# Kernel optimization log

Hardware: AMD Instinct MI355X
Metric: run time of the kernel (lower is better)

The kernel has to match this reference:

```python
import jax, jax.numpy as jnp
import numpy as np


def setup_inputs() -> dict:
    key = jax.random.key(0)
    k0, k1, k2, k3 = jax.random.split(key, 4)
    B, N, C, Dout = 4, 8192, 64, 128
    coords = jax.random.normal(k0, (B, N, 3), dtype=jnp.float32)
    features = jax.random.normal(k1, (B, N, C), dtype=jnp.float32)
    W1 = jax.random.normal(k2, (C + 3, Dout), dtype=jnp.float32) / jnp.sqrt(jnp.float32(C + 3))
    b1 = jnp.zeros((Dout,), dtype=jnp.float32)
    W2 = jax.random.normal(k3, (Dout, Dout), dtype=jnp.float32) / jnp.sqrt(jnp.float32(Dout))
    b2 = jnp.zeros((Dout,), dtype=jnp.float32)
    return {"coords": coords, "features": features, "W1": W1, "b1": b1,
            "W2": W2, "b2": b2, "sample_count": 2048, "k": 32}


def reference(coords, features, W1, b1, W2, b2, sample_count, k):
    B, N, _ = coords.shape
    S = min(sample_count, N)
    kk = min(k, N)
    # deterministic linspace centroid sampling (same indices for every batch)
    idx = jnp.round(jnp.linspace(0.0, N - 1, S)).astype(jnp.int32)  # [S]
    sampled = coords[:, idx]  # [B,S,3]
    # squared distances via GEMM (same topk ordering as torch.cdist)
    s2 = jnp.sum(sampled * sampled, axis=-1)          # [B,S]
    c2 = jnp.sum(coords * coords, axis=-1)            # [B,N]
    d2 = s2[:, :, None] + c2[:, None, :] - 2.0 * jnp.einsum('bsd,bnd->bsn', sampled, coords)
    _, knn_idx = jax.lax.top_k(-d2, kk)               # [B,S,kk] smallest distances
    # per-batch irregular gathers
    grouped_c = jax.vmap(lambda c, i: c[i])(coords, knn_idx)      # [B,S,kk,3]
    rel = grouped_c - sampled[:, :, None, :]                      # relative coords
    grouped_f = jax.vmap(lambda f, i: f[i])(features, knn_idx)    # [B,S,kk,C]
    g = jnp.concatenate([rel, grouped_f], axis=-1)                # [B,S,kk,C+3]
    # shared MLP: Linear -> GELU(exact) -> Linear -> GELU(exact)
    h = jax.nn.gelu(g @ W1 + b1, approximate=False)
    h = jax.nn.gelu(h @ W2 + b2, approximate=False)
    pooled = jnp.max(h, axis=2)                                   # [B,S,Dout]
    return sampled, pooled
```

## Files before the change

kernel.cpp:

```cpp
#include <hip/hip_runtime.h>
#include <math.h>

typedef unsigned int u32;
typedef unsigned long long u64;

#define BB 4
#define NN 8192
#define CC 64
#define DOUT 128
#define SS 2048
#define KSEL 32
#define CAPL 2048
#define CAP2 384
#define BREAK_CAP 128
#define GSTR 36

__device__ __forceinline__ int sample_index(int s) {
    if (s == 1706) return 6826;
    const double step = 8191.0 / 2047.0;
    return (int)rint((double)s * step);
}

__device__ __forceinline__ u32 f2s(float f) {
    u32 u = __float_as_uint(f);
    return ((int)u < 0) ? ~u : (u ^ 0x80000000u);
}

__device__ __forceinline__ float gelu(float x) {
    return 0.5f * x * (1.0f + erff(x * 0.70710678118654752f));
}

__global__ __launch_bounds__(256, 8) void k_select(const float* __restrict__ coords,
                                                   float* __restrict__ out_sampled,
                                                   int* __restrict__ selbuf,
                                                   int selstride) {
    __shared__ __align__(16) u64 cand[CAPL];
    __shared__ __align__(16) u64 cand2[CAP2];
    __shared__ u32 wsum[32];
    __shared__ int sel[KSEL];
    __shared__ int s_nsel, s_ncand, s_n2;

    const int tid = threadIdx.x;
    const int lane = tid & 63;
    const int q = blockIdx.x;
    const int b = q >> 11;
    const int s = q & (SS - 1);
    const int si = sample_index(s);

    const float* cb = coords + (size_t)b * NN * 3;
    const float qx = cb[si * 3 + 0], qy = cb[si * 3 + 1], qz = cb[si * 3 + 2];
    const float q2 = __fadd_rn(__fadd_rn(__fmul_rn(qx, qx), __fmul_rn(qy, qy)), __fmul_rn(qz, qz));

    if (tid == 0) {
        float* dst = out_sampled + (size_t)q * 3;
        dst[0] = qx; dst[1] = qy; dst[2] = qz;
    }

    u32 kr[32];
#pragma unroll
    for (int i = 0; i < 32; i++) {
        int j = tid + (i << 8);
        float x = cb[j * 3 + 0], y = cb[j * 3 + 1], z = cb[j * 3 + 2];
        float n2 = __fadd_rn(__fadd_rn(__fmul_rn(x, x), __fmul_rn(y, y)), __fmul_rn(z, z));
        float dot = __fadd_rn(__fadd_rn(__fmul_rn(qx, x), __fmul_rn(qy, y)), __fmul_rn(qz, z));
        float d2 = __fsub_rn(__fadd_rn(q2, n2), __fmul_rn(2.0f, dot));
        kr[i] = f2s(d2);
    }

#define BFLY_WSUM()                                                          \
    _Pragma("unroll")                                                        \
    for (int w = 0; w < 8; w++) {                                            \
        _Pragma("unroll")                                                    \
        for (int d = 1; d < 64; d <<= 1) cnt[w] += __shfl_xor(cnt[w], d, 64);\
    }                                                                        \
    if ((tid & 63) == 0) {                                                   \
        int wv = tid >> 6;                                                   \
        _Pragma("unroll")                                                    \
        for (int w = 0; w < 8; w++) wsum[wv * 8 + w] = cnt[w];               \
    }                                                                        \
    __syncthreads();

#define SCAN_DIGIT()                                                         \
    u32 tot[8];                                                              \
    _Pragma("unroll")                                                        \
    for (int w = 0; w < 8; w++)                                              \
        tot[w] = wsum[w] + wsum[8 + w] + wsum[16 + w] + wsum[24 + w];        \
    run = 0; D = 15; cc = 0;                                                 \
    _Pragma("unroll")                                                        \
    for (int nib = 0; nib < 16; nib++) {                                     \
        int cv = (nib & 1) ? (int)(tot[nib >> 1] >> 16)                      \
                           : (int)(tot[nib >> 1] & 0xFFFFu);                 \
        if (base + run + cv >= KSEL) { D = nib; cc = cv; break; }            \
        run += cv;                                                           \
    }

    u32 pref = 0;
    int base = 0, shift = 28, c = 0;
    int p = 7;
    {
        u32 cnt[8] = {0, 0, 0, 0, 0, 0, 0, 0};
#pragma unroll
        for (int i = 0; i < 32; i++) {
            u32 nib = kr[i] >> 28;
            cnt[nib >> 1] += 1u << (16 * (nib & 1));
        }
        BFLY_WSUM()
        int run, D, cc;
        SCAN_DIGIT()
        base = run; pref = (u32)D << 28; c = cc;
        __syncthreads();
    }

    while (c > CAPL && p > 0) {
        p--;
        const int sh = 4 * p;
        const u32 hmask = 0xFFFFFFFFu << (sh + 4);
        u32 cnt[8] = {0, 0, 0, 0, 0, 0, 0, 0};
#pragma unroll
        for (int i = 0; i < 32; i++) {
            u32 kv = kr[i];
            if ((kv & hmask) == pref) {
                u32 nib = (kv >> sh) & 15u;
                cnt[nib >> 1] += 1u << (16 * (nib & 1));
            }
        }
        BFLY_WSUM()
        int run, D, cc;
        SCAN_DIGIT()
        base += run; pref |= (u32)D << sh; shift = sh; c = cc;
        __syncthreads();
    }

    if (tid == 0) { s_nsel = 0; s_ncand = 0; }
    __syncthreads();

    const u64 lmlt = (1ull << lane) - 1ull;
    {
        const u32 prefv = pref >> shift;
#pragma unroll
        for (int i = 0; i < 32; i++) {
            int j = tid + (i << 8);
            u32 kv = kr[i];
            u32 kp = kv >> shift;
            bool isS = kp < prefv;
            bool isC = kp == prefv;
            u64 bs = __ballot(isS);
            u64 bc = __ballot(isC);
            int basS = 0, basC = 0;
            if (lane == 0) {
                if (bs) basS = atomicAdd(&s_nsel, (int)__popcll(bs));
                if (bc) basC = atomicAdd(&s_ncand, (int)__popcll(bc));
            }
            basS = __shfl(basS, 0, 64);
            basC = __shfl(basC, 0, 64);
            if (isS) sel[basS + (int)__popcll(bs & lmlt)] = j;
            if (isC) {
                int pos = basC + (int)__popcll(bc & lmlt);
                if (pos < CAPL) cand[pos] = ((u64)kv << 32) | (u32)j;
            }
        }
    }
    __syncthreads();
    int nc = s_ncand; if (nc > CAPL) nc = CAPL;

    int p2 = shift >> 2;
    while (c > BREAK_CAP && p2 > 0) {
        p2--;
        const int sh = 4 * p2;
        const u32 ph = pref >> (sh + 4);
        u32 cnt[8] = {0, 0, 0, 0, 0, 0, 0, 0};
        for (int e = tid; e < nc; e += 256) {
            u32 kv = (u32)(cand[e] >> 32);
            if ((kv >> (sh + 4)) == ph) {
                u32 nib = (kv >> sh) & 15u;
                cnt[nib >> 1] += 1u << (16 * (nib & 1));
            }
        }
        BFLY_WSUM()
        int run, D, cc;
        SCAN_DIGIT()
        base += run; pref |= (u32)D << sh; shift = sh; c = cc;
        __syncthreads();
    }
#undef BFLY_WSUM
#undef SCAN_DIGIT

    if (tid == 0) s_n2 = 0;
    __syncthreads();
    {
        const u32 pv = pref >> shift;
        for (int e = tid; e < nc; e += 256) {
            u64 ent = cand[e];
            u32 kp = (u32)(ent >> 32) >> shift;
            bool isS = kp < pv;
            bool isC = kp == pv;
            u64 bs = __ballot(isS);
            u64 bc = __ballot(isC);
            int basS = 0, basC = 0;
            if (lane == 0) {
                if (bs) basS = atomicAdd(&s_nsel, (int)__popcll(bs));
                if (bc) basC = atomicAdd(&s_n2, (int)__popcll(bc));
            }
            basS = __shfl(basS, 0, 64);
            basC = __shfl(basC, 0, 64);
            if (isS) sel[basS + (int)__popcll(bs & lmlt)] = (int)(ent & 0xFFFFFFFFu);
            if (isC) {
                int pos = basC + (int)__popcll(bc & lmlt);
                if (pos < CAP2) cand2[pos] = ent;
            }
        }
    }
    __syncthreads();

    {
        const int nles = s_nsel;
        const int need = KSEL - nles;
        int n2 = s_n2; if (n2 > CAP2) n2 = CAP2;
        for (int ci = tid; ci < n2; ci += 256) {
            u64 me = cand2[ci];
            int r = 0;
            for (int m = 0; m < n2; m++) r += (cand2[m] < me) ? 1 : 0;
            if (r < need) sel[nles + r] = (int)(me & 0xFFFFFFFFu);
        }
    }
    __syncthreads();

    if (tid < KSEL) selbuf[(size_t)q * selstride + tid] = sel[tid];
}

__global__ __launch_bounds__(256, 8) void k_mlp(const float* __restrict__ coords,
                                                const float* __restrict__ features,
                                                const float* __restrict__ w1,
                                                const float* __restrict__ b1,
                                                const float* __restrict__ w2,
                                                const float* __restrict__ b2,
                                                const int* __restrict__ selbuf,
                                                int selstride,
                                                float* __restrict__ pooled) {
    __shared__ __align__(16) unsigned char smem[18432];
    float* g = (float*)smem;
    float* h = (float*)smem;
    __shared__ int sel[KSEL];

    const int tid = threadIdx.x;
    const int q = blockIdx.x;
    const int b = q >> 11;
    const int s = q & (SS - 1);
    const int si = sample_index(s);

    const float* cb = coords + (size_t)b * NN * 3;
    const float qx = cb[si * 3 + 0], qy = cb[si * 3 + 1], qz = cb[si * 3 + 2];

    if (tid < KSEL) sel[tid] = selbuf[(size_t)q * selstride + tid];
    __syncthreads();

    {
        const int gi = tid >> 3;
        const int gc = tid & 7;
        const int n = sel[gi];
        const float* fb = features + ((size_t)b * NN + n) * CC;
#pragma unroll
        for (int m = 0; m < 9; m++) {
            int c = gc + (m << 3);
            if (c < 67) {
                float v;
                if (c < 3) v = cb[n * 3 + c] - ((c == 0) ? qx : (c == 1) ? qy : qz);
                else       v = fb[c - 3];
                g[c * GSTR + gi] = v;
            }
        }
    }
    __syncthreads();

    const int jg  = tid >> 2;
    const int inb = tid & 3;
    const int n0  = inb << 3;
    const int j0  = jg << 1;

    float acc0[8], acc1[8];

    {
        float2 bb = *(const float2*)(b1 + j0);
#pragma unroll
        for (int t = 0; t < 8; t++) { acc0[t] = bb.x; acc1[t] = bb.y; }
        const float* w1p = w1 + j0;
        for (int c = 0; c < 67; c++) {
            float2 wv = *(const float2*)(w1p + c * DOUT);
            const float* gr = g + c * GSTR + n0;
            float4 p0 = *(const float4*)(gr);
            float4 p1 = *(const float4*)(gr + 4);
            float a[8] = {p0.x, p0.y, p0.z, p0.w, p1.x, p1.y, p1.z, p1.w};
#pragma unroll
            for (int t = 0; t < 8; t++) {
                acc0[t] = fmaf(a[t], wv.x, acc0[t]);
                acc1[t] = fmaf(a[t], wv.y, acc1[t]);
            }
        }
    }
    __syncthreads();
    {
        float* h0 = h + (size_t)j0 * GSTR + n0;
        float* h1 = h0 + GSTR;
        float4 v0 = {gelu(acc0[0]), gelu(acc0[1]), gelu(acc0[2]), gelu(acc0[3])};
        float4 v1 = {gelu(acc0[4]), gelu(acc0[5]), gelu(acc0[6]), gelu(acc0[7])};
        *(float4*)(h0)     = v0;
        *(float4*)(h0 + 4) = v1;
        float4 v2 = {gelu(acc1[0]), gelu(acc1[1]), gelu(acc1[2]), gelu(acc1[3])};
        float4 v3 = {gelu(acc1[4]), gelu(acc1[5]), gelu(acc1[6]), gelu(acc1[7])};
        *(float4*)(h1)     = v2;
        *(float4*)(h1 + 4) = v3;
    }
    __syncthreads();

    {
        float2 bb = *(const float2*)(b2 + j0);
#pragma unroll
        for (int t = 0; t < 8; t++) { acc0[t] = bb.x; acc1[t] = bb.y; }
        const float* w2p = w2 + j0;
        for (int c = 0; c < DOUT; c++) {
            float2 wv = *(const float2*)(w2p + c * DOUT);
            const float* hr = h + c * GSTR + n0;
            float4 p0 = *(const float4*)(hr);
            float4 p1 = *(const float4*)(hr + 4);
            float a[8] = {p0.x, p0.y, p0.z, p0.w, p1.x, p1.y, p1.z, p1.w};
#pragma unroll
            for (int t = 0; t < 8; t++) {
                acc0[t] = fmaf(a[t], wv.x, acc0[t]);
                acc1[t] = fmaf(a[t], wv.y, acc1[t]);
            }
        }
    }

    float m0 = gelu(acc0[0]);
    float m1 = gelu(acc1[0]);
#pragma unroll
    for (int t = 1; t < 8; t++) {
        m0 = fmaxf(m0, gelu(acc0[t]));
        m1 = fmaxf(m1, gelu(acc1[t]));
    }
#pragma unroll
    for (int d = 1; d < 4; d <<= 1) {
        m0 = fmaxf(m0, __shfl_xor(m0, d, 64));
        m1 = fmaxf(m1, __shfl_xor(m1, d, 64));
    }
    if (inb == 0) {
        float2 out = {m0, m1};
        *(float2*)(pooled + (size_t)q * DOUT + j0) = out;
    }
}

extern "C" void kernel_launch(void* const* d_in, const int* in_sizes, int n_in,
                              void* d_out, int out_size, void* d_ws, size_t ws_size,
                              hipStream_t stream) {
    const float* coords = nullptr;
    const float* features = nullptr;
    const float* W1 = nullptr;
    const float* b1 = nullptr;
    const float* W2 = nullptr;
    const float* b2 = nullptr;
    for (int i = 0; i < n_in; i++) {
        int sz = in_sizes[i];
        const float* p = (const float*)d_in[i];
        if      (sz == BB * NN * 3)     coords = p;
        else if (sz == BB * NN * CC)    features = p;
        else if (sz == (CC + 3) * DOUT) W1 = p;
        else if (sz == DOUT * DOUT)     W2 = p;
        else if (sz == DOUT)            { if (!b1) b1 = p; else b2 = p; }
    }

    float* out_sampled = (float*)d_out;
    float* out_pooled  = (float*)d_out + (size_t)BB * SS * 3;

    const size_t sel_bytes = (size_t)BB * SS * KSEL * sizeof(int);
    int* selbuf;
    int selstride;
    if (ws_size >= sel_bytes && d_ws != nullptr) {
        selbuf = (int*)d_ws;
        selstride = KSEL;
    } else {
        selbuf = (int*)out_pooled;
        selstride = DOUT;
    }

    k_select<<<dim3(BB * SS), dim3(256), 0, stream>>>(coords, out_sampled, selbuf, selstride);
    k_mlp<<<dim3(BB * SS), dim3(256), 0, stream>>>(coords, features, W1, b1, W2, b2,
                                                   selbuf, selstride, out_pooled);
}
```

Before: 472.6 us.

## Fuse kNN selection and MLP into one kernel with shared smem union

Merges the neighbor-selection kernel and the MLP kernel into a single kernel, so each block selects its 32 neighbors and then gathers and runs the two-layer MLP directly from shared memory. The intermediate index buffer, its global write/read round trip and one kernel launch are removed. Shared memory is unioned between the candidate arrays and the MLP tiles. The launch-bounds occupancy hint is dropped, which may change register allocation, and the combined kernel has higher register pressure, which can reduce occupancy and the overlap between the two phases across blocks.

```diff
diff --git a/kernel.cpp b/kernel.cpp
--- a/kernel.cpp
+++ b/kernel.cpp
@@ -30,12 +30,19 @@
     return 0.5f * x * (1.0f + erff(x * 0.70710678118654752f));
 }
 
-__global__ __launch_bounds__(256, 8) void k_select(const float* __restrict__ coords,
-                                                   float* __restrict__ out_sampled,
-                                                   int* __restrict__ selbuf,
-                                                   int selstride) {
-    __shared__ __align__(16) u64 cand[CAPL];
-    __shared__ __align__(16) u64 cand2[CAP2];
+__global__ __launch_bounds__(256) void k_fused(const float* __restrict__ coords,
+                                               const float* __restrict__ features,
+                                               const float* __restrict__ w1,
+                                               const float* __restrict__ b1,
+                                               const float* __restrict__ w2,
+                                               const float* __restrict__ b2,
+                                               float* __restrict__ out_sampled,
+                                               float* __restrict__ pooled) {
+    __shared__ __align__(16) unsigned char smem[19456];
+    u64*   cand  = (u64*)smem;
+    u64*   cand2 = (u64*)(smem + 16384);
+    float* g     = (float*)smem;
+    float* h     = (float*)smem;
     __shared__ u32 wsum[32];
     __shared__ int sel[KSEL];
     __shared__ int s_nsel, s_ncand, s_n2;
@@ -225,35 +232,6 @@
     }
     __syncthreads();
 
-    if (tid < KSEL) selbuf[(size_t)q * selstride + tid] = sel[tid];
-}
-
-__global__ __launch_bounds__(256, 8) void k_mlp(const float* __restrict__ coords,
-                                                const float* __restrict__ features,
-                                                const float* __restrict__ w1,
-                                                const float* __restrict__ b1,
-                                                const float* __restrict__ w2,
-                                                const float* __restrict__ b2,
-                                                const int* __restrict__ selbuf,
-                                                int selstride,
-                                                float* __restrict__ pooled) {
-    __shared__ __align__(16) unsigned char smem[18432];
-    float* g = (float*)smem;
-    float* h = (float*)smem;
-    __shared__ int sel[KSEL];
-
-    const int tid = threadIdx.x;
-    const int q = blockIdx.x;
-    const int b = q >> 11;
-    const int s = q & (SS - 1);
-    const int si = sample_index(s);
-
-    const float* cb = coords + (size_t)b * NN * 3;
-    const float qx = cb[si * 3 + 0], qy = cb[si * 3 + 1], qz = cb[si * 3 + 2];
-
-    if (tid < KSEL) sel[tid] = selbuf[(size_t)q * selstride + tid];
-    __syncthreads();
-
     {
         const int gi = tid >> 3;
         const int gc = tid & 7;
@@ -261,12 +239,12 @@
         const float* fb = features + ((size_t)b * NN + n) * CC;
 #pragma unroll
         for (int m = 0; m < 9; m++) {
-            int c = gc + (m << 3);
-            if (c < 67) {
+            int ch = gc + (m << 3);
+            if (ch < 67) {
                 float v;
-                if (c < 3) v = cb[n * 3 + c] - ((c == 0) ? qx : (c == 1) ? qy : qz);
-                else       v = fb[c - 3];
-                g[c * GSTR + gi] = v;
+                if (ch < 3) v = cb[n * 3 + ch] - ((ch == 0) ? qx : (ch == 1) ? qy : qz);
+                else        v = fb[ch - 3];
+                g[ch * GSTR + gi] = v;
             }
         }
     }
@@ -284,9 +262,9 @@
 #pragma unroll
         for (int t = 0; t < 8; t++) { acc0[t] = bb.x; acc1[t] = bb.y; }
         const float* w1p = w1 + j0;
-        for (int c = 0; c < 67; c++) {
-            float2 wv = *(const float2*)(w1p + c * DOUT);
-            const float* gr = g + c * GSTR + n0;
+        for (int ch = 0; ch < 67; ch++) {
+            float2 wv = *(const float2*)(w1p + ch * DOUT);
+            const float* gr = g + ch * GSTR + n0;
             float4 p0 = *(const float4*)(gr);
             float4 p1 = *(const float4*)(gr + 4);
             float a[8] = {p0.x, p0.y, p0.z, p0.w, p1.x, p1.y, p1.z, p1.w};
@@ -317,9 +295,9 @@
 #pragma unroll
         for (int t = 0; t < 8; t++) { acc0[t] = bb.x; acc1[t] = bb.y; }
         const float* w2p = w2 + j0;
-        for (int c = 0; c < DOUT; c++) {
-            float2 wv = *(const float2*)(w2p + c * DOUT);
-            const float* hr = h + c * GSTR + n0;
+        for (int ch = 0; ch < DOUT; ch++) {
+            float2 wv = *(const float2*)(w2p + ch * DOUT);
+            const float* hr = h + ch * GSTR + n0;
             float4 p0 = *(const float4*)(hr);
             float4 p1 = *(const float4*)(hr + 4);
             float a[8] = {p0.x, p0.y, p0.z, p0.w, p1.x, p1.y, p1.z, p1.w};
@@ -371,18 +349,6 @@
     float* out_sampled = (float*)d_out;
     float* out_pooled  = (float*)d_out + (size_t)BB * SS * 3;
 
-    const size_t sel_bytes = (size_t)BB * SS * KSEL * sizeof(int);
-    int* selbuf;
-    int selstride;
-    if (ws_size >= sel_bytes && d_ws != nullptr) {
-        selbuf = (int*)d_ws;
-        selstride = KSEL;
-    } else {
-        selbuf = (int*)out_pooled;
-        selstride = DOUT;
-    }
-
-    k_select<<<dim3(BB * SS), dim3(256), 0, stream>>>(coords, out_sampled, selbuf, selstride);
-    k_mlp<<<dim3(BB * SS), dim3(256), 0, stream>>>(coords, features, W1, b1, W2, b2,
-                                                   selbuf, selstride, out_pooled);
-}
+    k_fused<<<dim3(BB * SS), dim3(256), 0, stream>>>(coords, features, W1, b1, W2, b2,
+                                                     out_sampled, out_pooled);
+}
```

New measurement: 492.7 us. 4.2% more time.

## Restructure MLP kernel: two queries per block, per-wave uniform weight columns

Applied to the files above, without the earlier changes.

The MLP kernel now handles two sampled queries per block. Each wave owns 32 output channels, chosen with a wave-uniform readfirstlane so the weight rows can be read as scalar broadcast loads, and each lane owns one neighbor with 32 accumulators. Max-pooling moves from shuffles to a swizzled shared-memory transpose followed by a per-channel reduction. This is meant to cut redundant vector weight loads and LDS traffic per FMA, at the cost of more registers (occupancy hint dropped), more shared memory per block and an extra pooling pass.

```diff
diff --git a/kernel.cpp b/kernel.cpp
--- a/kernel.cpp
+++ b/kernel.cpp
@@ -13,7 +13,6 @@
 #define CAPL 2048
 #define CAP2 384
 #define BREAK_CAP 128
-#define GSTR 36
 
 __device__ __forceinline__ int sample_index(int s) {
     if (s == 1706) return 6826;
@@ -228,124 +227,118 @@
     if (tid < KSEL) selbuf[(size_t)q * selstride + tid] = sel[tid];
 }
 
-__global__ __launch_bounds__(256, 8) void k_mlp(const float* __restrict__ coords,
-                                                const float* __restrict__ features,
-                                                const float* __restrict__ w1,
-                                                const float* __restrict__ b1,
-                                                const float* __restrict__ w2,
-                                                const float* __restrict__ b2,
-                                                const int* __restrict__ selbuf,
-                                                int selstride,
-                                                float* __restrict__ pooled) {
-    __shared__ __align__(16) unsigned char smem[18432];
-    float* g = (float*)smem;
-    float* h = (float*)smem;
-    __shared__ int sel[KSEL];
+__global__ __launch_bounds__(256) void k_mlp(const float* __restrict__ coords,
+                                             const float* __restrict__ features,
+                                             const float* __restrict__ w1,
+                                             const float* __restrict__ b1,
+                                             const float* __restrict__ w2,
+                                             const float* __restrict__ b2,
+                                             const int* __restrict__ selbuf,
+                                             int selstride,
+                                             float* __restrict__ pooled) {
+    __shared__ __align__(16) unsigned char smem[32768];
+    float* g    = (float*)smem;
+    float* h    = (float*)smem;
+    float* part = (float*)smem;
+    __shared__ int sel2[2][KSEL];
 
     const int tid = threadIdx.x;
-    const int q = blockIdx.x;
-    const int b = q >> 11;
-    const int s = q & (SS - 1);
-    const int si = sample_index(s);
-
+    const int q0 = blockIdx.x << 1;
+    const int b = q0 >> 11;
     const float* cb = coords + (size_t)b * NN * 3;
-    const float qx = cb[si * 3 + 0], qy = cb[si * 3 + 1], qz = cb[si * 3 + 2];
-
-    if (tid < KSEL) sel[tid] = selbuf[(size_t)q * selstride + tid];
-    __syncthreads();
-
-    {
-        const int gi = tid >> 3;
-        const int gc = tid & 7;
-        const int n = sel[gi];
+
+    if (tid < 2 * KSEL) {
+        int hq = tid >> 5;
+        sel2[hq][tid & 31] = selbuf[(size_t)(q0 + hq) * selstride + (tid & 31)];
+    }
+    __syncthreads();
+
+    {
+        const int hq = tid >> 7;
+        const int s = (q0 + hq) & (SS - 1);
+        const int si = sample_index(s);
+        const float qx = cb[si * 3 + 0], qy = cb[si * 3 + 1], qz = cb[si * 3 + 2];
+        const int nbr = (tid >> 2) & 31;
+        const int cl = tid & 3;
+        const int n = sel2[hq][nbr];
         const float* fb = features + ((size_t)b * NN + n) * CC;
-#pragma unroll
-        for (int m = 0; m < 9; m++) {
-            int c = gc + (m << 3);
-            if (c < 67) {
+        float* gq = g + hq * 2144;
+#pragma unroll
+        for (int m = 0; m < 17; m++) {
+            int ch = cl + (m << 2);
+            if (ch < 67) {
                 float v;
-                if (c < 3) v = cb[n * 3 + c] - ((c == 0) ? qx : (c == 1) ? qy : qz);
-                else       v = fb[c - 3];
-                g[c * GSTR + gi] = v;
-            }
-        }
-    }
-    __syncthreads();
-
-    const int jg  = tid >> 2;
-    const int inb = tid & 3;
-    const int n0  = inb << 3;
-    const int j0  = jg << 1;
-
-    float acc0[8], acc1[8];
-
-    {
-        float2 bb = *(const float2*)(b1 + j0);
-#pragma unroll
-        for (int t = 0; t < 8; t++) { acc0[t] = bb.x; acc1[t] = bb.y; }
-        const float* w1p = w1 + j0;
+                if (ch < 3) v = cb[n * 3 + ch] - ((ch == 0) ? qx : (ch == 1) ? qy : qz);
+                else        v = fb[ch - 3];
+                gq[ch * 32 + nbr] = v;
+            }
+        }
+    }
+    __syncthreads();
+
+    const int lane = tid & 63;
+    const int chb = __builtin_amdgcn_readfirstlane((tid >> 6) << 5);
+    const int hq = lane >> 5;
+    const int nb = lane & 31;
+
+    float acc[32];
+
+    {
+        const float* brow = b1 + chb;
+#pragma unroll
+        for (int k = 0; k < 32; k++) acc[k] = brow[k];
+        const float* aA = g + hq * 2144 + nb;
+        const float* w1p = w1 + chb;
         for (int c = 0; c < 67; c++) {
-            float2 wv = *(const float2*)(w1p + c * DOUT);
-            const float* gr = g + c * GSTR + n0;
-            float4 p0 = *(const float4*)(gr);
-            float4 p1 = *(const float4*)(gr + 4);
-            float a[8] = {p0.x, p0.y, p0.z, p0.w, p1.x, p1.y, p1.z, p1.w};
-#pragma unroll
-            for (int t = 0; t < 8; t++) {
-                acc0[t] = fmaf(a[t], wv.x, acc0[t]);
-                acc1[t] = fmaf(a[t], wv.y, acc1[t]);
-            }
-        }
-    }
-    __syncthreads();
-    {
-        float* h0 = h + (size_t)j0 * GSTR + n0;
-        float* h1 = h0 + GSTR;
-        float4 v0 = {gelu(acc0[0]), gelu(acc0[1]), gelu(acc0[2]), gelu(acc0[3])};
-        float4 v1 = {gelu(acc0[4]), gelu(acc0[5]), gelu(acc0[6]), gelu(acc0[7])};
-        *(float4*)(h0)     = v0;
-        *(float4*)(h0 + 4) = v1;
-        float4 v2 = {gelu(acc1[0]), gelu(acc1[1]), gelu(acc1[2]), gelu(acc1[3])};
-        float4 v3 = {gelu(acc1[4]), gelu(acc1[5]), gelu(acc1[6]), gelu(acc1[7])};
-        *(float4*)(h1)     = v2;
-        *(float4*)(h1 + 4) = v3;
-    }
-    __syncthreads();
-
-    {
-        float2 bb = *(const float2*)(b2 + j0);
-#pragma unroll
-        for (int t = 0; t < 8; t++) { acc0[t] = bb.x; acc1[t] = bb.y; }
-        const float* w2p = w2 + j0;
+            float a = aA[c * 32];
+            const float* wr = w1p + c * DOUT;
+#pragma unroll
+            for (int k = 0; k < 32; k++) acc[k] = fmaf(a, wr[k], acc[k]);
+        }
+    }
+    __syncthreads();
+    {
+        float* hp = h + hq * 4096 + nb;
+#pragma unroll
+        for (int k = 0; k < 32; k++) hp[(chb + k) * 32] = gelu(acc[k]);
+    }
+    __syncthreads();
+
+    {
+        const float* brow = b2 + chb;
+#pragma unroll
+        for (int k = 0; k < 32; k++) acc[k] = brow[k];
+        const float* aA = h + hq * 4096 + nb;
+        const float* w2p = w2 + chb;
         for (int c = 0; c < DOUT; c++) {
-            float2 wv = *(const float2*)(w2p + c * DOUT);
-            const float* hr = h + c * GSTR + n0;
-            float4 p0 = *(const float4*)(hr);
-            float4 p1 = *(const float4*)(hr + 4);
-            float a[8] = {p0.x, p0.y, p0.z, p0.w, p1.x, p1.y, p1.z, p1.w};
-#pragma unroll
-            for (int t = 0; t < 8; t++) {
-                acc0[t] = fmaf(a[t], wv.x, acc0[t]);
-                acc1[t] = fmaf(a[t], wv.y, acc1[t]);
-            }
-        }
-    }
-
-    float m0 = gelu(acc0[0]);
-    float m1 = gelu(acc1[0]);
-#pragma unroll
-    for (int t = 1; t < 8; t++) {
-        m0 = fmaxf(m0, gelu(acc0[t]));
-        m1 = fmaxf(m1, gelu(acc1[t]));
-    }
-#pragma unroll
-    for (int d = 1; d < 4; d <<= 1) {
-        m0 = fmaxf(m0, __shfl_xor(m0, d, 64));
-        m1 = fmaxf(m1, __shfl_xor(m1, d, 64));
-    }
-    if (inb == 0) {
-        float2 out = {m0, m1};
-        *(float2*)(pooled + (size_t)q * DOUT + j0) = out;
+            float a = aA[c * 32];
+            const float* wr = w2p + c * DOUT;
+#pragma unroll
+            for (int k = 0; k < 32; k++) acc[k] = fmaf(a, wr[k], acc[k]);
+        }
+    }
+#pragma unroll
+    for (int k = 0; k < 32; k++) acc[k] = gelu(acc[k]);
+    __syncthreads();
+    {
+        float* pp = part + hq * 4096;
+#pragma unroll
+        for (int k = 0; k < 32; k++) {
+            int j = chb + k;
+            pp[j * 32 + (nb ^ (j & 31))] = acc[k];
+        }
+    }
+    __syncthreads();
+
+    {
+        const int hq2 = tid >> 7;
+        const int ch = tid & 127;
+        const float* pr = part + hq2 * 4096 + ch * 32;
+        const int sw = ch & 31;
+        float m = pr[0 ^ sw];
+#pragma unroll
+        for (int w = 1; w < 32; w++) m = fmaxf(m, pr[w ^ sw]);
+        pooled[(size_t)(q0 + hq2) * DOUT + ch] = m;
     }
 }
 
@@ -383,6 +376,6 @@
     }
 
     k_select<<<dim3(BB * SS), dim3(256), 0, stream>>>(coords, out_sampled, selbuf, selstride);
-    k_mlp<<<dim3(BB * SS), dim3(256), 0, stream>>>(coords, features, W1, b1, W2, b2,
-                                                   selbuf, selstride, out_pooled);
-}
+    k_mlp<<<dim3((BB * SS) / 2), dim3(256), 0, stream>>>(coords, features, W1, b1, W2, b2,
+                                                         selbuf, selstride, out_pooled);
+}
```

New measurement: 465.3 us. Within noise of the previous version (-1.5%).
